# Kernel tuning notes

Hardware: AMD Instinct MI355X
Metric: run time of the kernel (lower is better)

## Reference

```python
import jax, jax.numpy as jnp
import numpy as np

COL_DIM = 4096   # number of rows of x (feature dim for cols_layers SAGEConv)
ROW_DIM = 1024   # number of cols of x (feature dim for rows_layers SAGEConv)
NUM_LAYERS = 3
KNN_E = 16384    # edges over the ROW_DIM nodes of x.T
GENET_E = 131072 # edges over the COL_DIM nodes of x


def setup_inputs() -> dict:
    key = jax.random.key(0)
    ks = jax.random.split(key, 10)
    s = 0.02
    x = jax.random.normal(ks[0], (COL_DIM, ROW_DIM), jnp.float32)
    knn_edge_index = jax.random.randint(ks[1], (2, KNN_E), 0, ROW_DIM, dtype=jnp.int32)
    genet_edge_index = jax.random.randint(ks[2], (2, GENET_E), 0, COL_DIM, dtype=jnp.int32)
    col_Wl = jax.random.normal(ks[3], (NUM_LAYERS, COL_DIM, COL_DIM), jnp.float32) * s
    col_Wr = jax.random.normal(ks[4], (NUM_LAYERS, COL_DIM, COL_DIM), jnp.float32) * s
    col_b  = jax.random.normal(ks[5], (NUM_LAYERS, COL_DIM), jnp.float32) * s
    row_Wl = jax.random.normal(ks[6], (NUM_LAYERS, ROW_DIM, ROW_DIM), jnp.float32) * s
    row_Wr = jax.random.normal(ks[7], (NUM_LAYERS, ROW_DIM, ROW_DIM), jnp.float32) * s
    row_b  = jax.random.normal(ks[8], (NUM_LAYERS, ROW_DIM), jnp.float32) * s
    return dict(x=x, col_Wl=col_Wl, col_Wr=col_Wr, col_b=col_b,
                row_Wl=row_Wl, row_Wr=row_Wr, row_b=row_b,
                knn_edge_index=knn_edge_index, genet_edge_index=genet_edge_index)


def _sage(x, src, dst, Wl, b, Wr, n):
    # PyG SAGEConv (aggr='mean', root_weight=True): lin_l(mean_neighbors) + lin_r(x)
    msg = x[src]                                                  # [E, d] gather
    agg = jax.ops.segment_sum(msg, dst, num_segments=n)           # [n, d] scatter-add
    cnt = jax.ops.segment_sum(jnp.ones((src.shape[0],), x.dtype), dst, num_segments=n)
    mean = agg / jnp.maximum(cnt, 1.0)[:, None]                   # mean with empty-neighbor guard
    return mean @ Wl.T + b + x @ Wr.T


def reference(x, col_Wl, col_Wr, col_b, row_Wl, row_Wr, row_b,
              knn_edge_index, genet_edge_index):
    # Dropout is identity in eval mode. LeakyReLU(inplace) makes both branch
    # orders reduce to leaky_relu(sage(x)) per layer.
    leaky = lambda v: jax.nn.leaky_relu(v, 0.01)
    ks, kd = knn_edge_index[0], knn_edge_index[1]
    gs, gd = genet_edge_index[0], genet_edge_index[1]
    e = x
    for i in range(NUM_LAYERS):
        e = leaky(_sage(e.T, ks, kd, col_Wl[i], col_b[i], col_Wr[i], ROW_DIM)).T
        e = leaky(_sage(e, gs, gd, row_Wl[i], row_b[i], row_Wr[i], COL_DIM))
    return e
```

## Files before the change

### kernel.cpp

```cpp
#include <hip/hip_runtime.h>

#define COL_DIM 4096
#define ROW_DIM 1024
#define NUM_LAYERS 3
#define KNN_E 16384
#define GENET_E 131072

typedef __attribute__((ext_vector_type(8))) _Float16 half8;
typedef __attribute__((ext_vector_type(2))) __fp16 fp16x2;
typedef __attribute__((ext_vector_type(4))) float f32x4;

__device__ inline unsigned short f2h(float f) {
  union { _Float16 h; unsigned short u; } c;
  c.h = (_Float16)f;
  return c.u;
}
__device__ inline unsigned int pkrtz(float a, float b) {
  union { fp16x2 p; unsigned int u; } c;
  c.p = __builtin_amdgcn_cvt_pkrtz(a, b);
  return c.u;
}
__device__ inline half8 cvt8h(float4 a, float4 b) {
  union { unsigned int u[4]; half8 v; } r;
  r.u[0] = pkrtz(a.x, a.y);
  r.u[1] = pkrtz(a.z, a.w);
  r.u[2] = pkrtz(b.x, b.y);
  r.u[3] = pkrtz(b.z, b.w);
  return r.v;
}

__global__ void transpose_split_kernel(const float* __restrict__ in,
                                       float* __restrict__ outf,
                                       unsigned short* __restrict__ outh,
                                       int R, int C) {
  __shared__ float tile[32][33];
  int c0 = blockIdx.x * 32, r0 = blockIdx.y * 32;
  int tx = threadIdx.x, ty = threadIdx.y;
#pragma unroll
  for (int i = 0; i < 32; i += 8)
    tile[ty + i][tx] = in[(size_t)(r0 + ty + i) * C + c0 + tx];
  __syncthreads();
#pragma unroll
  for (int i = 0; i < 32; i += 8) {
    float v = tile[tx][ty + i];
    size_t o = (size_t)(c0 + ty + i) * R + r0 + tx;
    outf[o] = v;
    outh[o] = f2h(v);
  }
}

__global__ void count_kernel(const int* __restrict__ dst, int E, int* __restrict__ cnt) {
  int e = blockIdx.x * 256 + threadIdx.x;
  if (e < E) atomicAdd(&cnt[dst[e]], 1);
}

__global__ void scan_kernel(const int* __restrict__ cnt, int* __restrict__ indptr, int n) {
  __shared__ int s[1024];
  __shared__ int base_s;
  int tid = threadIdx.x;
  if (tid == 0) { base_s = 0; indptr[0] = 0; }
  __syncthreads();
  for (int c = 0; c < n; c += 1024) {
    int i = c + tid;
    int v = (i < n) ? cnt[i] : 0;
    s[tid] = v;
    __syncthreads();
    for (int off = 1; off < 1024; off <<= 1) {
      int t = (tid >= off) ? s[tid - off] : 0;
      __syncthreads();
      s[tid] += t;
      __syncthreads();
    }
    if (i < n) indptr[i + 1] = base_s + s[tid];
    __syncthreads();
    if (tid == 0) base_s += s[1023];
    __syncthreads();
  }
}

__global__ void copy_int_kernel(const int* __restrict__ a, int* __restrict__ b, int n) {
  int i = blockIdx.x * 256 + threadIdx.x;
  if (i < n) b[i] = a[i];
}

__global__ void fill_kernel(const int* __restrict__ src, const int* __restrict__ dst, int E,
                            int* __restrict__ cursor, int* __restrict__ idx) {
  int e = blockIdx.x * 256 + threadIdx.x;
  if (e < E) {
    int p = atomicAdd(&cursor[dst[e]], 1);
    idx[p] = src[e];
  }
}

__global__ void rank_sort_kernel(const int* __restrict__ indptr, int* __restrict__ idx,
                                 int n) {
  int wv = threadIdx.x >> 6, lane = threadIdx.x & 63;
  int b = blockIdx.x * (blockDim.x >> 6) + wv;
  if (b >= n) return;
  int lo = indptr[b];
  int d = indptr[b + 1] - lo;
  if (d <= 1) return;
  if (d <= 256) {
    int v0 = (lane < d) ? idx[lo + lane] : 0x7fffffff;
    int v1 = (64 + lane < d) ? idx[lo + 64 + lane] : 0x7fffffff;
    int v2 = (128 + lane < d) ? idx[lo + 128 + lane] : 0x7fffffff;
    int v3 = (192 + lane < d) ? idx[lo + 192 + lane] : 0x7fffffff;
    int r0 = 0, r1 = 0, r2 = 0, r3 = 0;
    for (int j = 0; j < d; j++) {
      int q = j >> 6;
      int sel = (q == 0) ? v0 : (q == 1) ? v1 : (q == 2) ? v2 : v3;
      int bj = __shfl(sel, j & 63);
      r0 += (bj < v0 || (bj == v0 && j < lane)) ? 1 : 0;
      r1 += (bj < v1 || (bj == v1 && j < 64 + lane)) ? 1 : 0;
      r2 += (bj < v2 || (bj == v2 && j < 128 + lane)) ? 1 : 0;
      r3 += (bj < v3 || (bj == v3 && j < 192 + lane)) ? 1 : 0;
    }
    if (lane < d) idx[lo + r0] = v0;
    if (64 + lane < d) idx[lo + r1] = v1;
    if (128 + lane < d) idx[lo + r2] = v2;
    if (192 + lane < d) idx[lo + r3] = v3;
  } else if (lane == 0) {
    for (int i = lo + 1; i < lo + d; i++) {
      int v = idx[i];
      int j = i - 1;
      while (j >= lo && idx[j] > v) { idx[j + 1] = idx[j]; j--; }
      idx[j + 1] = v;
    }
  }
}

__global__ void agg_slice_kernel(const float* __restrict__ src,
                                 unsigned short* __restrict__ dh,
                                 const int* __restrict__ indptr,
                                 const int* __restrict__ idx, int D, int tprsh) {
  int tid = threadIdx.x;
  int d = blockIdx.y * (256 >> tprsh) + (tid >> tprsh);
  int k4 = blockIdx.x * (1 << tprsh) + (tid & ((1 << tprsh) - 1));
  int lo = indptr[d], hi = indptr[d + 1];
  float4 s = make_float4(0.f, 0.f, 0.f, 0.f);
  for (int j = lo; j < hi; j++) {
    float4 v = ((const float4*)(src + (size_t)idx[j] * D))[k4];
    s.x += v.x; s.y += v.y; s.z += v.z; s.w += v.w;
  }
  int c = hi - lo;
  float inv = 1.f / (float)(c > 0 ? c : 1);
  s.x *= inv; s.y *= inv; s.z *= inv; s.w *= inv;
  ushort4 h;
  h.x = f2h(s.x); h.y = f2h(s.y); h.z = f2h(s.z); h.w = f2h(s.w);
  ((ushort4*)(dh + (size_t)d * D))[k4] = h;
}

#define GBM 128
#define GBN 128
#define GBK 32

#define GLDS(g, l)                                                             \
  __builtin_amdgcn_global_load_lds(                                            \
      (const __attribute__((address_space(1))) void*)(g),                      \
      (__attribute__((address_space(3))) void*)(l), 16, 0, 0)

#define BAR()                                                                  \
  {                                                                            \
    asm volatile("" ::: "memory");                                             \
    __builtin_amdgcn_s_barrier();                                              \
    asm volatile("" ::: "memory");                                             \
  }

template <int AF32>
__global__ __launch_bounds__(256, 2) void dual_gemm_kernel(
    const float* __restrict__ Wf1, const float* __restrict__ Wf2,
    const unsigned short* __restrict__ Xh1, const unsigned short* __restrict__ Xh2,
    float* __restrict__ P0, float* __restrict__ P1, int Kloc) {
  __shared__ char smraw[2][24576];
  const int tid = threadIdx.x;
  const int lane = tid & 63;
  const int wid = tid >> 6;
  const int wr = wid >> 1, wc = wid & 1;

  const int bid = blockIdx.x;
  const int kh = bid >> 8;
  const int tile = bid & 255;
  const int swz = (tile & 7) * 32 + (tile >> 3);
  const int bm0 = (swz >> 3) * GBM;
  const int bn0 = (swz & 7) * GBN;

  const float* Wf = kh ? Wf2 : Wf1;
  const unsigned short* Xh = kh ? Xh2 : Xh1;
  const size_t wrow = AF32 ? (size_t)bm0 : (size_t)bn0;
  const size_t xrow = AF32 ? (size_t)bn0 : (size_t)bm0;

  const int u0 = tid, u1 = tid + 256, u2 = tid + 512, u3 = tid + 768;
  const int fr0 = u0 >> 3, fr1 = u1 >> 3, fr2 = u2 >> 3, fr3 = u3 >> 3;
  const int fc0 = ((u0 & 7) ^ (fr0 & 7)) * 4;
  const int fc1 = ((u1 & 7) ^ (fr1 & 7)) * 4;
  const int fc2 = ((u2 & 7) ^ (fr2 & 7)) * 4;
  const int fc3 = ((u3 & 7) ^ (fr3 & 7)) * 4;
  const float* gF0 = Wf + (wrow + fr0) * Kloc + fc0;
  const float* gF1 = Wf + (wrow + fr1) * Kloc + fc1;
  const float* gF2 = Wf + (wrow + fr2) * Kloc + fc2;
  const float* gF3 = Wf + (wrow + fr3) * Kloc + fc3;
  const int hr0 = u0 >> 2, hr1 = u1 >> 2;
  const int hc0 = ((u0 & 3) ^ ((hr0 >> 1) & 3)) * 8;
  const int hc1 = ((u1 & 3) ^ ((hr1 >> 1) & 3)) * 8;
  const unsigned short* gH0 = Xh + (xrow + hr0) * Kloc + hc0;
  const unsigned short* gH1 = Xh + (xrow + hr1) * Kloc + hc1;

#define STAGE(buf)                                                             \
  {                                                                            \
    char* base = &smraw[buf][0];                                               \
    GLDS(gF0, base + u0 * 16); GLDS(gF1, base + u1 * 16);                      \
    GLDS(gF2, base + u2 * 16); GLDS(gF3, base + u3 * 16);                      \
    GLDS(gH0, base + 16384 + u0 * 16); GLDS(gH1, base + 16384 + u1 * 16);      \
    gF0 += GBK; gF1 += GBK; gF2 += GBK; gF3 += GBK;                            \
    gH0 += GBK; gH1 += GBK;                                                    \
  }

  int offH[4];
  int offF[4][2];
  {
    int s = lane >> 4;
#pragma unroll
    for (int i = 0; i < 4; i++) {
      int rh = (AF32 ? wc : wr) * 64 + i * 16 + (lane & 15);
      offH[i] = rh * 32 + ((s ^ ((rh >> 1) & 3)) * 8);
      int rf = (AF32 ? wr : wc) * 64 + i * 16 + (lane & 15);
      offF[i][0] = rf * 32 + (((2 * s) ^ (rf & 7)) * 4);
      offF[i][1] = rf * 32 + (((2 * s + 1) ^ (rf & 7)) * 4);
    }
  }

  f32x4 acc[4][4];
#pragma unroll
  for (int i = 0; i < 4; i++)
#pragma unroll
    for (int j = 0; j < 4; j++) acc[i][j] = (f32x4)(0.f);

  const int nt = Kloc / GBK;
  STAGE(0);
  STAGE(1);
  int cur = 0;
  for (int t = 0; t < nt; t++) {
    if (t < nt - 1) {
      asm volatile("s_waitcnt vmcnt(6)" ::: "memory");
    } else {
      asm volatile("s_waitcnt vmcnt(0)" ::: "memory");
    }
    BAR();
    const float* smF = (const float*)&smraw[cur][0];
    const unsigned short* smH = (const unsigned short*)&smraw[cur][16384];
    half8 cw[4], rd[4];
#pragma unroll
    for (int i = 0; i < 4; i++) {
      float4 a = *(const float4*)&smF[offF[i][0]];
      float4 b = *(const float4*)&smF[offF[i][1]];
      cw[i] = cvt8h(a, b);
      rd[i] = *(const half8*)&smH[offH[i]];
    }
    __builtin_amdgcn_s_setprio(1);
    if constexpr (AF32) {
#pragma unroll
      for (int i = 0; i < 4; i++)
#pragma unroll
        for (int j = 0; j < 4; j++)
          acc[i][j] = __builtin_amdgcn_mfma_f32_16x16x32_f16(cw[i], rd[j],
                                                             acc[i][j], 0, 0, 0);
    } else {
#pragma unroll
      for (int i = 0; i < 4; i++)
#pragma unroll
        for (int j = 0; j < 4; j++)
          acc[i][j] = __builtin_amdgcn_mfma_f32_16x16x32_f16(rd[i], cw[j],
                                                             acc[i][j], 0, 0, 0);
    }
    __builtin_amdgcn_s_setprio(0);
    BAR();
    if (t + 2 < nt) STAGE(cur);
    cur ^= 1;
  }

  float* P = kh ? P1 : P0;
  const int rowq = (lane >> 4) * 4;
  const int colq = lane & 15;
#pragma unroll
  for (int i = 0; i < 4; i++) {
#pragma unroll
    for (int j = 0; j < 4; j++) {
#pragma unroll
      for (int e = 0; e < 4; e++) {
        int row = bm0 + wr * 64 + i * 16 + rowq + e;
        int col = bn0 + wc * 64 + j * 16 + colq;
        P[(size_t)row * 1024 + col] = acc[i][j][e];
      }
    }
  }
}

__global__ void combine_split_kernel(const float* __restrict__ P0, const float* __restrict__ P1,
                                     const float* __restrict__ bias, float* __restrict__ Cf,
                                     unsigned short* __restrict__ Ch) {
  int i = blockIdx.x * 256 + threadIdx.x;
  float4 a = ((const float4*)P0)[i];
  float4 b = ((const float4*)P1)[i];
  float bb = bias[(i * 4) >> 10];
  float4 v;
  v.x = a.x + b.x + bb;
  v.y = a.y + b.y + bb;
  v.z = a.z + b.z + bb;
  v.w = a.w + b.w + bb;
  v.x = v.x > 0.f ? v.x : 0.01f * v.x;
  v.y = v.y > 0.f ? v.y : 0.01f * v.y;
  v.z = v.z > 0.f ? v.z : 0.01f * v.z;
  v.w = v.w > 0.f ? v.w : 0.01f * v.w;
  ((float4*)Cf)[i] = v;
  ushort4 h;
  h.x = f2h(v.x); h.y = f2h(v.y); h.z = f2h(v.z); h.w = f2h(v.w);
  ((ushort4*)Ch)[i] = h;
}

__global__ void combine_kernel(const float* __restrict__ P0, const float* __restrict__ P1,
                               const float* __restrict__ bias, float* __restrict__ C) {
  int i = blockIdx.x * 256 + threadIdx.x;
  float4 a = ((const float4*)P0)[i];
  float4 b = ((const float4*)P1)[i];
  float4 bb = *(const float4*)(bias + ((i * 4) & 1023));
  float4 v;
  v.x = a.x + b.x + bb.x;
  v.y = a.y + b.y + bb.y;
  v.z = a.z + b.z + bb.z;
  v.w = a.w + b.w + bb.w;
  v.x = v.x > 0.f ? v.x : 0.01f * v.x;
  v.y = v.y > 0.f ? v.y : 0.01f * v.y;
  v.z = v.z > 0.f ? v.z : 0.01f * v.z;
  v.w = v.w > 0.f ? v.w : 0.01f * v.w;
  ((float4*)C)[i] = v;
}

extern "C" void kernel_launch(void* const* d_in, const int* in_sizes, int n_in,
                              void* d_out, int out_size, void* d_ws, size_t ws_size,
                              hipStream_t stream) {
  const float* x      = (const float*)d_in[0];
  const float* col_Wl = (const float*)d_in[1];
  const float* col_Wr = (const float*)d_in[2];
  const float* col_b  = (const float*)d_in[3];
  const float* row_Wl = (const float*)d_in[4];
  const float* row_Wr = (const float*)d_in[5];
  const float* row_b  = (const float*)d_in[6];
  const int*   knn    = (const int*)d_in[7];
  const int*   genet  = (const int*)d_in[8];
  float* out = (float*)d_out;

  const size_t MAT = (size_t)COL_DIM * ROW_DIM;
  char* w = (char*)d_ws;
  float* ET  = (float*)w; w += MAT * 4;
  float* E1  = (float*)w; w += MAT * 4;
  unsigned short* ETh = (unsigned short*)w; w += MAT * 2;
  unsigned short* Mh  = (unsigned short*)w; w += MAT * 2;
  unsigned short* Gh  = (unsigned short*)w; w += MAT * 2;
  unsigned short* E1h = (unsigned short*)w; w += MAT * 2;
  float* PP0 = (float*)w; w += MAT * 4;
  float* PP1 = (float*)w; w += MAT * 4;
  int* kcnt = (int*)w; w += 1024 * 4;
  int* kptr = (int*)w; w += 1025 * 4;
  int* kidx = (int*)w; w += KNN_E * 4;
  int* gcnt = (int*)w; w += 4096 * 4;
  int* gptr = (int*)w; w += 4097 * 4;
  int* gidx = (int*)w; w += (size_t)GENET_E * 4;

  hipMemsetAsync(kcnt, 0, 1024 * 4, stream);
  hipMemsetAsync(gcnt, 0, 4096 * 4, stream);
  count_kernel<<<KNN_E / 256, 256, 0, stream>>>(knn + KNN_E, KNN_E, kcnt);
  count_kernel<<<GENET_E / 256, 256, 0, stream>>>(genet + GENET_E, GENET_E, gcnt);
  scan_kernel<<<1, 1024, 0, stream>>>(kcnt, kptr, 1024);
  scan_kernel<<<1, 1024, 0, stream>>>(gcnt, gptr, 4096);
  copy_int_kernel<<<4, 256, 0, stream>>>(kptr, kcnt, 1024);
  copy_int_kernel<<<16, 256, 0, stream>>>(gptr, gcnt, 4096);
  fill_kernel<<<KNN_E / 256, 256, 0, stream>>>(knn, knn + KNN_E, KNN_E, kcnt, kidx);
  fill_kernel<<<GENET_E / 256, 256, 0, stream>>>(genet, genet + GENET_E, GENET_E, gcnt, gidx);
  rank_sort_kernel<<<256, 256, 0, stream>>>(kptr, kidx, 1024);
  rank_sort_kernel<<<1024, 256, 0, stream>>>(gptr, gidx, 4096);

  const float* Ein = x;
  for (int i = 0; i < NUM_LAYERS; i++) {
    const float* cWl = col_Wl + (size_t)i * COL_DIM * COL_DIM;
    const float* cWr = col_Wr + (size_t)i * COL_DIM * COL_DIM;
    const float* cb  = col_b + (size_t)i * COL_DIM;
    const float* rWl = row_Wl + (size_t)i * ROW_DIM * ROW_DIM;
    const float* rWr = row_Wr + (size_t)i * ROW_DIM * ROW_DIM;
    const float* rb  = row_b + (size_t)i * ROW_DIM;

    transpose_split_kernel<<<dim3(ROW_DIM / 32, COL_DIM / 32), dim3(32, 8), 0, stream>>>(
        Ein, ET, ETh, COL_DIM, ROW_DIM);
    agg_slice_kernel<<<dim3(8, 512), 256, 0, stream>>>(ET, Mh, kptr, kidx,
                                                       COL_DIM, 7);
    dual_gemm_kernel<1><<<512, 256, 0, stream>>>(
        cWl, cWr, Mh, ETh, PP0, PP1, COL_DIM);
    combine_split_kernel<<<4096, 256, 0, stream>>>(PP0, PP1, cb, E1, E1h);

    agg_slice_kernel<<<dim3(8, 512), 256, 0, stream>>>(E1, Gh, gptr, gidx,
                                                       ROW_DIM, 5);
    dual_gemm_kernel<0><<<512, 256, 0, stream>>>(
        rWl, rWr, Gh, E1h, PP0, PP1, ROW_DIM);
    combine_kernel<<<4096, 256, 0, stream>>>(PP0, PP1, rb, out);

    Ein = out;
  }
}
```

Measured before the change: 886.7 us.

## Pre-convert weights to fp16 and split-K the dual GEMM into four partials

```diff
diff --git a/kernel.cpp b/kernel.cpp
--- a/kernel.cpp
+++ b/kernel.cpp
@@ -7,26 +7,12 @@
 #define GENET_E 131072
 
 typedef __attribute__((ext_vector_type(8))) _Float16 half8;
-typedef __attribute__((ext_vector_type(2))) __fp16 fp16x2;
 typedef __attribute__((ext_vector_type(4))) float f32x4;
 
 __device__ inline unsigned short f2h(float f) {
   union { _Float16 h; unsigned short u; } c;
   c.h = (_Float16)f;
   return c.u;
-}
-__device__ inline unsigned int pkrtz(float a, float b) {
-  union { fp16x2 p; unsigned int u; } c;
-  c.p = __builtin_amdgcn_cvt_pkrtz(a, b);
-  return c.u;
-}
-__device__ inline half8 cvt8h(float4 a, float4 b) {
-  union { unsigned int u[4]; half8 v; } r;
-  r.u[0] = pkrtz(a.x, a.y);
-  r.u[1] = pkrtz(a.z, a.w);
-  r.u[2] = pkrtz(b.x, b.y);
-  r.u[3] = pkrtz(b.z, b.w);
-  return r.v;
 }
 
 __global__ void transpose_split_kernel(const float* __restrict__ in,
@@ -46,6 +32,18 @@
     size_t o = (size_t)(c0 + ty + i) * R + r0 + tx;
     outf[o] = v;
     outh[o] = f2h(v);
+  }
+}
+
+__global__ void split_f16_kernel(const float* __restrict__ src,
+                                 unsigned short* __restrict__ dh, int n4) {
+  int i = blockIdx.x * 256 + threadIdx.x;
+  int stride = gridDim.x * 256;
+  for (; i < n4; i += stride) {
+    float4 v = ((const float4*)src)[i];
+    ushort4 h;
+    h.x = f2h(v.x); h.y = f2h(v.y); h.z = f2h(v.z); h.w = f2h(v.w);
+    ((ushort4*)dh)[i] = h;
   }
 }
 
@@ -166,66 +164,54 @@
     asm volatile("" ::: "memory");                                             \
   }
 
-template <int AF32>
-__global__ __launch_bounds__(256, 2) void dual_gemm_kernel(
-    const float* __restrict__ Wf1, const float* __restrict__ Wf2,
-    const unsigned short* __restrict__ Xh1, const unsigned short* __restrict__ Xh2,
-    float* __restrict__ P0, float* __restrict__ P1, int Kloc) {
-  __shared__ char smraw[2][24576];
+__global__ __launch_bounds__(256, 4) void dual_gemm_kernel(
+    const unsigned short* __restrict__ A1, const unsigned short* __restrict__ A2,
+    const unsigned short* __restrict__ B1, const unsigned short* __restrict__ B2,
+    float* __restrict__ P0, float* __restrict__ P1,
+    float* __restrict__ P2, float* __restrict__ P3, int Ktot, int Kblk) {
+  __shared__ unsigned short sm[2][2][4096];
   const int tid = threadIdx.x;
   const int lane = tid & 63;
   const int wid = tid >> 6;
   const int wr = wid >> 1, wc = wid & 1;
 
   const int bid = blockIdx.x;
-  const int kh = bid >> 8;
-  const int tile = bid & 255;
-  const int swz = (tile & 7) * 32 + (tile >> 3);
-  const int bm0 = (swz >> 3) * GBM;
-  const int bn0 = (swz & 7) * GBN;
-
-  const float* Wf = kh ? Wf2 : Wf1;
-  const unsigned short* Xh = kh ? Xh2 : Xh1;
-  const size_t wrow = AF32 ? (size_t)bm0 : (size_t)bn0;
-  const size_t xrow = AF32 ? (size_t)bn0 : (size_t)bm0;
-
-  const int u0 = tid, u1 = tid + 256, u2 = tid + 512, u3 = tid + 768;
-  const int fr0 = u0 >> 3, fr1 = u1 >> 3, fr2 = u2 >> 3, fr3 = u3 >> 3;
-  const int fc0 = ((u0 & 7) ^ (fr0 & 7)) * 4;
-  const int fc1 = ((u1 & 7) ^ (fr1 & 7)) * 4;
-  const int fc2 = ((u2 & 7) ^ (fr2 & 7)) * 4;
-  const int fc3 = ((u3 & 7) ^ (fr3 & 7)) * 4;
-  const float* gF0 = Wf + (wrow + fr0) * Kloc + fc0;
-  const float* gF1 = Wf + (wrow + fr1) * Kloc + fc1;
-  const float* gF2 = Wf + (wrow + fr2) * Kloc + fc2;
-  const float* gF3 = Wf + (wrow + fr3) * Kloc + fc3;
-  const int hr0 = u0 >> 2, hr1 = u1 >> 2;
-  const int hc0 = ((u0 & 3) ^ ((hr0 >> 1) & 3)) * 8;
-  const int hc1 = ((u1 & 3) ^ ((hr1 >> 1) & 3)) * 8;
-  const unsigned short* gH0 = Xh + (xrow + hr0) * Kloc + hc0;
-  const unsigned short* gH1 = Xh + (xrow + hr1) * Kloc + hc1;
+  const int swz = (bid & 7) * 128 + (bid >> 3);
+  const int q = swz >> 8;
+  const int p = q >> 1, kh = q & 1;
+  const int tile = swz & 255;
+  const int bm0 = (tile >> 3) * GBM;
+  const int bn0 = (tile & 7) * GBN;
+  const size_t kbase = (size_t)kh * Kblk;
+
+  const unsigned short* A = p ? A2 : A1;
+  const unsigned short* B = p ? B2 : B1;
+
+  const int u0 = tid, u1 = tid + 256;
+  const int r0 = u0 >> 2, r1 = u1 >> 2;
+  const int c0 = ((u0 & 3) ^ ((r0 >> 1) & 3)) * 8;
+  const int c1 = ((u1 & 3) ^ ((r1 >> 1) & 3)) * 8;
+  const unsigned short* gA0 = A + (size_t)(bm0 + r0) * Ktot + kbase + c0;
+  const unsigned short* gA1 = A + (size_t)(bm0 + r1) * Ktot + kbase + c1;
+  const unsigned short* gB0 = B + (size_t)(bn0 + r0) * Ktot + kbase + c0;
+  const unsigned short* gB1 = B + (size_t)(bn0 + r1) * Ktot + kbase + c1;
 
 #define STAGE(buf)                                                             \
   {                                                                            \
-    char* base = &smraw[buf][0];                                               \
-    GLDS(gF0, base + u0 * 16); GLDS(gF1, base + u1 * 16);                      \
-    GLDS(gF2, base + u2 * 16); GLDS(gF3, base + u3 * 16);                      \
-    GLDS(gH0, base + 16384 + u0 * 16); GLDS(gH1, base + 16384 + u1 * 16);      \
-    gF0 += GBK; gF1 += GBK; gF2 += GBK; gF3 += GBK;                            \
-    gH0 += GBK; gH1 += GBK;                                                    \
-  }
-
-  int offH[4];
-  int offF[4][2];
+    GLDS(gA0, &sm[buf][0][u0 * 8]); GLDS(gA1, &sm[buf][0][u1 * 8]);            \
+    GLDS(gB0, &sm[buf][1][u0 * 8]); GLDS(gB1, &sm[buf][1][u1 * 8]);            \
+    gA0 += GBK; gA1 += GBK; gB0 += GBK; gB1 += GBK;                            \
+  }
+
+  int offA[4], offB[4];
   {
     int s = lane >> 4;
 #pragma unroll
     for (int i = 0; i < 4; i++) {
-      int rh = (AF32 ? wc : wr) * 64 + i * 16 + (lane & 15);
-      offH[i] = rh * 32 + ((s ^ ((rh >> 1) & 3)) * 8);
-      int rf = (AF32 ? wr : wc) * 64 + i * 16 + (lane & 15);
-      offF[i][0] = rf * 32 + (((2 * s) ^ (rf & 7)) * 4);
-      offF[i][1] = rf * 32 + (((2 * s + 1) ^ (rf & 7)) * 4);
+      int rA = wr * 64 + i * 16 + (lane & 15);
+      offA[i] = rA * 32 + ((s ^ ((rA >> 1) & 3)) * 8);
+      int rB = wc * 64 + i * 16 + (lane & 15);
+      offB[i] = rB * 32 + ((s ^ ((rB >> 1) & 3)) * 8);
     }
   }
 
@@ -235,50 +221,39 @@
 #pragma unroll
     for (int j = 0; j < 4; j++) acc[i][j] = (f32x4)(0.f);
 
-  const int nt = Kloc / GBK;
+  const int nt = Kblk / GBK;
   STAGE(0);
   STAGE(1);
   int cur = 0;
   for (int t = 0; t < nt; t++) {
     if (t < nt - 1) {
-      asm volatile("s_waitcnt vmcnt(6)" ::: "memory");
+      asm volatile("s_waitcnt vmcnt(4)" ::: "memory");
     } else {
       asm volatile("s_waitcnt vmcnt(0)" ::: "memory");
     }
     BAR();
-    const float* smF = (const float*)&smraw[cur][0];
-    const unsigned short* smH = (const unsigned short*)&smraw[cur][16384];
-    half8 cw[4], rd[4];
+    const unsigned short* smA = &sm[cur][0][0];
+    const unsigned short* smB = &sm[cur][1][0];
+    half8 av[4], bv[4];
 #pragma unroll
     for (int i = 0; i < 4; i++) {
-      float4 a = *(const float4*)&smF[offF[i][0]];
-      float4 b = *(const float4*)&smF[offF[i][1]];
-      cw[i] = cvt8h(a, b);
-      rd[i] = *(const half8*)&smH[offH[i]];
+      av[i] = *(const half8*)&smA[offA[i]];
+      bv[i] = *(const half8*)&smB[offB[i]];
     }
     __builtin_amdgcn_s_setprio(1);
-    if constexpr (AF32) {
-#pragma unroll
-      for (int i = 0; i < 4; i++)
-#pragma unroll
-        for (int j = 0; j < 4; j++)
-          acc[i][j] = __builtin_amdgcn_mfma_f32_16x16x32_f16(cw[i], rd[j],
-                                                             acc[i][j], 0, 0, 0);
-    } else {
-#pragma unroll
-      for (int i = 0; i < 4; i++)
-#pragma unroll
-        for (int j = 0; j < 4; j++)
-          acc[i][j] = __builtin_amdgcn_mfma_f32_16x16x32_f16(rd[i], cw[j],
-                                                             acc[i][j], 0, 0, 0);
-    }
+#pragma unroll
+    for (int i = 0; i < 4; i++)
+#pragma unroll
+      for (int j = 0; j < 4; j++)
+        acc[i][j] = __builtin_amdgcn_mfma_f32_16x16x32_f16(av[i], bv[j],
+                                                           acc[i][j], 0, 0, 0);
     __builtin_amdgcn_s_setprio(0);
     BAR();
     if (t + 2 < nt) STAGE(cur);
     cur ^= 1;
   }
 
-  float* P = kh ? P1 : P0;
+  float* P = q == 0 ? P0 : q == 1 ? P1 : q == 2 ? P2 : P3;
   const int rowq = (lane >> 4) * 4;
   const int colq = lane & 15;
 #pragma unroll
@@ -296,17 +271,20 @@
 }
 
 __global__ void combine_split_kernel(const float* __restrict__ P0, const float* __restrict__ P1,
+                                     const float* __restrict__ P2, const float* __restrict__ P3,
                                      const float* __restrict__ bias, float* __restrict__ Cf,
                                      unsigned short* __restrict__ Ch) {
   int i = blockIdx.x * 256 + threadIdx.x;
   float4 a = ((const float4*)P0)[i];
   float4 b = ((const float4*)P1)[i];
+  float4 c = ((const float4*)P2)[i];
+  float4 d = ((const float4*)P3)[i];
   float bb = bias[(i * 4) >> 10];
   float4 v;
-  v.x = a.x + b.x + bb;
-  v.y = a.y + b.y + bb;
-  v.z = a.z + b.z + bb;
-  v.w = a.w + b.w + bb;
+  v.x = a.x + b.x + c.x + d.x + bb;
+  v.y = a.y + b.y + c.y + d.y + bb;
+  v.z = a.z + b.z + c.z + d.z + bb;
+  v.w = a.w + b.w + c.w + d.w + bb;
   v.x = v.x > 0.f ? v.x : 0.01f * v.x;
   v.y = v.y > 0.f ? v.y : 0.01f * v.y;
   v.z = v.z > 0.f ? v.z : 0.01f * v.z;
@@ -318,16 +296,19 @@
 }
 
 __global__ void combine_kernel(const float* __restrict__ P0, const float* __restrict__ P1,
+                               const float* __restrict__ P2, const float* __restrict__ P3,
                                const float* __restrict__ bias, float* __restrict__ C) {
   int i = blockIdx.x * 256 + threadIdx.x;
   float4 a = ((const float4*)P0)[i];
   float4 b = ((const float4*)P1)[i];
+  float4 c = ((const float4*)P2)[i];
+  float4 d = ((const float4*)P3)[i];
   float4 bb = *(const float4*)(bias + ((i * 4) & 1023));
   float4 v;
-  v.x = a.x + b.x + bb.x;
-  v.y = a.y + b.y + bb.y;
-  v.z = a.z + b.z + bb.z;
-  v.w = a.w + b.w + bb.w;
+  v.x = a.x + b.x + c.x + d.x + bb.x;
+  v.y = a.y + b.y + c.y + d.y + bb.y;
+  v.z = a.z + b.z + c.z + d.z + bb.z;
+  v.w = a.w + b.w + c.w + d.w + bb.w;
   v.x = v.x > 0.f ? v.x : 0.01f * v.x;
   v.y = v.y > 0.f ? v.y : 0.01f * v.y;
   v.z = v.z > 0.f ? v.z : 0.01f * v.z;
@@ -350,6 +331,8 @@
   float* out = (float*)d_out;
 
   const size_t MAT = (size_t)COL_DIM * ROW_DIM;
+  const size_t WCOL = (size_t)COL_DIM * COL_DIM;
+  const size_t WROW = (size_t)ROW_DIM * ROW_DIM;
   char* w = (char*)d_ws;
   float* ET  = (float*)w; w += MAT * 4;
   float* E1  = (float*)w; w += MAT * 4;
@@ -357,8 +340,14 @@
   unsigned short* Mh  = (unsigned short*)w; w += MAT * 2;
   unsigned short* Gh  = (unsigned short*)w; w += MAT * 2;
   unsigned short* E1h = (unsigned short*)w; w += MAT * 2;
+  unsigned short* WH1 = (unsigned short*)w; w += WCOL * 2;
+  unsigned short* WH2 = (unsigned short*)w; w += WCOL * 2;
+  unsigned short* RH1 = (unsigned short*)w; w += WROW * 2;
+  unsigned short* RH2 = (unsigned short*)w; w += WROW * 2;
   float* PP0 = (float*)w; w += MAT * 4;
   float* PP1 = (float*)w; w += MAT * 4;
+  float* PP2 = (float*)w; w += MAT * 4;
+  float* PP3 = (float*)w; w += MAT * 4;
   int* kcnt = (int*)w; w += 1024 * 4;
   int* kptr = (int*)w; w += 1025 * 4;
   int* kidx = (int*)w; w += KNN_E * 4;
@@ -381,26 +370,30 @@
 
   const float* Ein = x;
   for (int i = 0; i < NUM_LAYERS; i++) {
-    const float* cWl = col_Wl + (size_t)i * COL_DIM * COL_DIM;
-    const float* cWr = col_Wr + (size_t)i * COL_DIM * COL_DIM;
+    const float* cWl = col_Wl + (size_t)i * WCOL;
+    const float* cWr = col_Wr + (size_t)i * WCOL;
     const float* cb  = col_b + (size_t)i * COL_DIM;
-    const float* rWl = row_Wl + (size_t)i * ROW_DIM * ROW_DIM;
-    const float* rWr = row_Wr + (size_t)i * ROW_DIM * ROW_DIM;
+    const float* rWl = row_Wl + (size_t)i * WROW;
+    const float* rWr = row_Wr + (size_t)i * WROW;
     const float* rb  = row_b + (size_t)i * ROW_DIM;
 
     transpose_split_kernel<<<dim3(ROW_DIM / 32, COL_DIM / 32), dim3(32, 8), 0, stream>>>(
         Ein, ET, ETh, COL_DIM, ROW_DIM);
     agg_slice_kernel<<<dim3(8, 512), 256, 0, stream>>>(ET, Mh, kptr, kidx,
                                                        COL_DIM, 7);
-    dual_gemm_kernel<1><<<512, 256, 0, stream>>>(
-        cWl, cWr, Mh, ETh, PP0, PP1, COL_DIM);
-    combine_split_kernel<<<4096, 256, 0, stream>>>(PP0, PP1, cb, E1, E1h);
+    split_f16_kernel<<<2048, 256, 0, stream>>>(cWl, WH1, (int)(WCOL / 4));
+    split_f16_kernel<<<2048, 256, 0, stream>>>(cWr, WH2, (int)(WCOL / 4));
+    dual_gemm_kernel<<<1024, 256, 0, stream>>>(
+        WH1, WH2, Mh, ETh, PP0, PP1, PP2, PP3, COL_DIM, COL_DIM / 2);
+    combine_split_kernel<<<4096, 256, 0, stream>>>(PP0, PP1, PP2, PP3, cb, E1, E1h);
 
     agg_slice_kernel<<<dim3(8, 512), 256, 0, stream>>>(E1, Gh, gptr, gidx,
                                                        ROW_DIM, 5);
-    dual_gemm_kernel<0><<<512, 256, 0, stream>>>(
-        rWl, rWr, Gh, E1h, PP0, PP1, ROW_DIM);
-    combine_kernel<<<4096, 256, 0, stream>>>(PP0, PP1, rb, out);
+    split_f16_kernel<<<1024, 256, 0, stream>>>(rWl, RH1, (int)(WROW / 4));
+    split_f16_kernel<<<1024, 256, 0, stream>>>(rWr, RH2, (int)(WROW / 4));
+    dual_gemm_kernel<<<1024, 256, 0, stream>>>(
+        Gh, E1h, RH1, RH2, PP0, PP1, PP2, PP3, ROW_DIM, ROW_DIM / 2);
+    combine_kernel<<<4096, 256, 0, stream>>>(PP0, PP1, PP2, PP3, rb, out);
 
     Ein = out;
   }
```

After: 804.0 us. 1.1x faster.
